# Kernel optimization log

Measured on AMD Instinct MI355X. Metric: run time of the kernel, lower is better.

The kernel has to match this reference:

```python
import jax, jax.numpy as jnp
import numpy as np

D_MODEL = 768
NUM_HEADS = 12
HEAD_DIM = D_MODEL // NUM_HEADS

def setup_inputs() -> dict:
    key = jax.random.key(0)
    ks = jax.random.split(key, 7)
    B, S = 2, 4096
    q = jax.random.normal(ks[0], (B, S, D_MODEL), dtype=jnp.float32)
    k = jax.random.normal(ks[1], (B, S, D_MODEL), dtype=jnp.float32)
    v = jax.random.normal(ks[2], (B, S, D_MODEL), dtype=jnp.float32)
    # nn.Linear(d, d, bias=False): weight [out, in], y = x @ W.T
    s = 1.0 / np.sqrt(D_MODEL)
    W_q = jax.random.uniform(ks[3], (D_MODEL, D_MODEL), jnp.float32, -s, s)
    W_k = jax.random.uniform(ks[4], (D_MODEL, D_MODEL), jnp.float32, -s, s)
    W_v = jax.random.uniform(ks[5], (D_MODEL, D_MODEL), jnp.float32, -s, s)
    W_o = jax.random.uniform(ks[6], (D_MODEL, D_MODEL), jnp.float32, -s, s)
    return {"query": q, "key": k, "value": v,
            "W_q": W_q, "W_k": W_k, "W_v": W_v, "W_o": W_o}

def reference(query, key, value, W_q, W_k, W_v, W_o):
    B, S, _ = query.shape
    H, Dh = NUM_HEADS, HEAD_DIM
    scale = np.sqrt(Dh).astype(np.float32)

    def proj(x, W):  # x [B,S,D] -> [B,H,S,Dh]
        y = jnp.einsum('bsd,ed->bse', x, W)
        return y.reshape(B, S, H, Dh).transpose(0, 2, 1, 3)

    Q = proj(query, W_q)
    K = proj(key, W_k)
    V = proj(value, W_v)
    scores = jnp.einsum('bhqd,bhkd->bhqk', Q, K) / scale
    attn = jax.nn.softmax(scores, axis=-1)  # dropout p=0 -> identity (eval)
    out = jnp.einsum('bhqk,bhkd->bhqd', attn, V)
    out = out.transpose(0, 2, 1, 3).reshape(B, S, H * Dh)
    return jnp.einsum('bsd,ed->bse', out, W_o)
```

## Files before the change

kernel.cpp:

```cpp
#include <hip/hip_runtime.h>

#define D_MODEL 768
#define S_LEN   4096
#define NHEAD   12
#define HDIM    64
#define BATCH   2
#define M_ROWS  (BATCH * S_LEN)

typedef __bf16    bf16x8 __attribute__((ext_vector_type(8)));
typedef float     f32x4  __attribute__((ext_vector_type(4)));
typedef float     f32x16 __attribute__((ext_vector_type(16)));
typedef unsigned  u32x4  __attribute__((ext_vector_type(4)));

#define QSCALE 0.18033688011f

__device__ __forceinline__ unsigned int bfb(float x) {
    return (unsigned int)__builtin_bit_cast(unsigned short, (__bf16)x);
}

__device__ __forceinline__ unsigned cvtpk(float lo, float hi) {
    unsigned r;
    asm("v_cvt_pk_bf16_f32 %0, %1, %2" : "=v"(r) : "v"(lo), "v"(hi));
    return r;
}

#if !__has_builtin(__builtin_amdgcn_exp2f)
extern "C" __device__ float __ocml_native_exp2_f32(float);
#endif
__device__ __forceinline__ float fexp2(float x) {
#if __has_builtin(__builtin_amdgcn_exp2f)
    return __builtin_amdgcn_exp2f(x);
#else
    return __ocml_native_exp2_f32(x);
#endif
}

__device__ __forceinline__ void gload16(const void* g, const void* l) {
    __builtin_amdgcn_global_load_lds(
        (const __attribute__((address_space(1))) unsigned int*)g,
        (__attribute__((address_space(3))) unsigned int*)l, 16, 0, 0);
}

#define MFMA16(a, b, c) __builtin_amdgcn_mfma_f32_16x16x32_bf16(a, b, c, 0, 0, 0)
#define MFMA32(a, b, c) __builtin_amdgcn_mfma_f32_32x32x16_bf16(a, b, c, 0, 0, 0)

__global__ __launch_bounds__(256)
void cvt_bf16(const float* __restrict__ s0, const float* __restrict__ s1,
              const float* __restrict__ s2, const float* __restrict__ s3,
              __bf16* __restrict__ d0, __bf16* __restrict__ d1,
              __bf16* __restrict__ d2, __bf16* __restrict__ d3, int n) {
    const int z = blockIdx.y;
    const float* s = z == 0 ? s0 : z == 1 ? s1 : z == 2 ? s2 : s3;
    __bf16*      d = z == 0 ? d0 : z == 1 ? d1 : z == 2 ? d2 : d3;
    const size_t i = ((size_t)blockIdx.x * 256 + threadIdx.x) * 8;
    if (i >= (size_t)n) return;
    float4 a = *(const float4*)(s + i);
    float4 b = *(const float4*)(s + i + 4);
    bf16x8 o;
    o[0] = (__bf16)a.x; o[1] = (__bf16)a.y; o[2] = (__bf16)a.z; o[3] = (__bf16)a.w;
    o[4] = (__bf16)b.x; o[5] = (__bf16)b.y; o[6] = (__bf16)b.z; o[7] = (__bf16)b.w;
    *(bf16x8*)(d + i) = o;
}

__global__ __launch_bounds__(256)
void mm_qkv(const __bf16* __restrict__ X0, const __bf16* __restrict__ X1,
            const __bf16* __restrict__ X2, const __bf16* __restrict__ W0,
            const __bf16* __restrict__ W1, const __bf16* __restrict__ W2,
            __bf16* __restrict__ C0q, __bf16* __restrict__ C1k,
            __bf16* __restrict__ C2v) {
    __shared__ __align__(16) char lds[24576];
    const int z = blockIdx.z;
    const __bf16* Xb = z == 0 ? X0 : z == 1 ? X1 : X2;
    const __bf16* Wb = z == 0 ? W0 : z == 1 ? W1 : W2;

    const int t    = threadIdx.x;
    const int w    = t >> 6;
    const int wr   = w >> 1, wc = w & 1;
    const int lane = t & 63;
    const int q15  = lane & 15;
    const int g    = lane >> 4;
    const int n0   = blockIdx.x * 64;
    const int m0   = blockIdx.y * 128;

    f32x4 acc[4][2];
#pragma unroll
    for (int i = 0; i < 4; i++)
#pragma unroll
        for (int j = 0; j < 2; j++) acc[i][j] = (f32x4){0.f, 0.f, 0.f, 0.f};

    const int srow  = lane >> 2;
    const int sslot = lane & 3;

#define MM_STAGE(B, K0)                                                        \
    {                                                                          \
        _Pragma("unroll")                                                      \
        for (int j = 0; j < 2; j++) {                                          \
            const int lrow = j * 64 + w * 16 + srow;                           \
            const int xs   = (lrow ^ (lrow >> 2)) & 3;                         \
            gload16(Xb + (size_t)(m0 + lrow) * D_MODEL + (K0) +                \
                        ((sslot ^ xs) << 3),                                   \
                    lds + (B) * 12288 + j * 4096 + w * 1024);                  \
        }                                                                      \
        {                                                                      \
            const int lrow = w * 16 + srow;                                    \
            const int xs   = (lrow ^ (lrow >> 2)) & 3;                         \
            gload16(Wb + (size_t)(n0 + lrow) * D_MODEL + (K0) +                \
                        ((sslot ^ xs) << 3),                                   \
                    lds + (B) * 12288 + 8192 + w * 1024);                      \
        }                                                                      \
    }

#define MM_COMPUTE(B)                                                          \
    {                                                                          \
        bf16x8 xa[4], wf[2];                                                   \
        _Pragma("unroll")                                                      \
        for (int mi = 0; mi < 4; mi++) {                                       \
            const int r  = wr * 64 + mi * 16 + q15;                            \
            const int sl = g ^ ((r ^ (r >> 2)) & 3);                           \
            xa[mi] = *(const bf16x8*)(lds + (B) * 12288 + r * 64 + sl * 16);   \
        }                                                                      \
        _Pragma("unroll")                                                      \
        for (int nj = 0; nj < 2; nj++) {                                       \
            const int r  = wc * 32 + nj * 16 + q15;                            \
            const int sl = g ^ ((r ^ (r >> 2)) & 3);                           \
            wf[nj] = *(const bf16x8*)(lds + (B) * 12288 + 8192 + r * 64 +      \
                                      sl * 16);                                \
        }                                                                      \
        _Pragma("unroll")                                                      \
        for (int mi = 0; mi < 4; mi++)                                         \
            _Pragma("unroll")                                                  \
            for (int nj = 0; nj < 2; nj++)                                     \
                acc[mi][nj] = MFMA16(xa[mi], wf[nj], acc[mi][nj]);             \
    }

    MM_STAGE(0, 0);
    __syncthreads();
#pragma unroll 1
    for (int ks = 0; ks < 24; ks += 2) {
        if (ks + 1 < 24) MM_STAGE(1, (ks + 1) * 32);
        MM_COMPUTE(0);
        __syncthreads();
        if (ks + 2 < 24) MM_STAGE(0, (ks + 2) * 32);
        MM_COMPUTE(1);
        __syncthreads();
    }
#undef MM_STAGE
#undef MM_COMPUTE

#pragma unroll
    for (int mi = 0; mi < 4; mi++) {
#pragma unroll
        for (int nj = 0; nj < 2; nj++) {
            const int n  = n0 + wc * 32 + nj * 16 + q15;
            const int mb = m0 + wr * 64 + mi * 16 + 4 * g;
            const int h = n >> 6, dh = n & 63;
            if (z == 0) {
#pragma unroll
                for (int r = 0; r < 4; r++) {
                    const int m = mb + r, b = m >> 12, s = m & 4095;
                    C0q[(((size_t)(b * NHEAD + h)) * S_LEN + s) * HDIM + dh] =
                        (__bf16)(acc[mi][nj][r] * QSCALE);
                }
            } else if (z == 1) {
#pragma unroll
                for (int r = 0; r < 4; r++) {
                    const int m = mb + r, b = m >> 12, s = m & 4095;
                    C1k[(((size_t)(b * NHEAD + h)) * S_LEN + s) * HDIM + dh] =
                        (__bf16)acc[mi][nj][r];
                }
            } else {
                const int b = mb >> 12, s = mb & 4095;
                uint2 pk;
                pk.x = bfb(acc[mi][nj][0]) | (bfb(acc[mi][nj][1]) << 16);
                pk.y = bfb(acc[mi][nj][2]) | (bfb(acc[mi][nj][3]) << 16);
                *(uint2*)(C2v +
                    (((size_t)(b * NHEAD + h)) * HDIM + dh) * S_LEN + s) = pk;
            }
        }
    }
}

__global__ __launch_bounds__(256)
void mm_out(const __bf16* __restrict__ Xb, const __bf16* __restrict__ Wb,
            float* __restrict__ C0) {
    __shared__ __align__(16) char lds[24576];
    const int t    = threadIdx.x;
    const int w    = t >> 6;
    const int wr   = w >> 1, wc = w & 1;
    const int lane = t & 63;
    const int q15  = lane & 15;
    const int g    = lane >> 4;
    const int n0   = blockIdx.x * 64;
    const int m0   = blockIdx.y * 128;

    f32x4 acc[4][2];
#pragma unroll
    for (int i = 0; i < 4; i++)
#pragma unroll
        for (int j = 0; j < 2; j++) acc[i][j] = (f32x4){0.f, 0.f, 0.f, 0.f};

    const int srow  = lane >> 2;
    const int sslot = lane & 3;

#define MM_STAGE(B, K0)                                                        \
    {                                                                          \
        _Pragma("unroll")                                                      \
        for (int j = 0; j < 2; j++) {                                          \
            const int lrow = j * 64 + w * 16 + srow;                           \
            const int xs   = (lrow ^ (lrow >> 2)) & 3;                         \
            gload16(Xb + (size_t)(m0 + lrow) * D_MODEL + (K0) +                \
                        ((sslot ^ xs) << 3),                                   \
                    lds + (B) * 12288 + j * 4096 + w * 1024);                  \
        }                                                                      \
        {                                                                      \
            const int lrow = w * 16 + srow;                                    \
            const int xs   = (lrow ^ (lrow >> 2)) & 3;                         \
            gload16(Wb + (size_t)(n0 + lrow) * D_MODEL + (K0) +                \
                        ((sslot ^ xs) << 3),                                   \
                    lds + (B) * 12288 + 8192 + w * 1024);                      \
        }                                                                      \
    }

#define MM_COMPUTE(B)                                                          \
    {                                                                          \
        bf16x8 xa[4], wf[2];                                                   \
        _Pragma("unroll")                                                      \
        for (int mi = 0; mi < 4; mi++) {                                       \
            const int r  = wr * 64 + mi * 16 + q15;                            \
            const int sl = g ^ ((r ^ (r >> 2)) & 3);                           \
            xa[mi] = *(const bf16x8*)(lds + (B) * 12288 + r * 64 + sl * 16);   \
        }                                                                      \
        _Pragma("unroll")                                                      \
        for (int nj = 0; nj < 2; nj++) {                                       \
            const int r  = wc * 32 + nj * 16 + q15;                            \
            const int sl = g ^ ((r ^ (r >> 2)) & 3);                           \
            wf[nj] = *(const bf16x8*)(lds + (B) * 12288 + 8192 + r * 64 +      \
                                      sl * 16);                                \
        }                                                                      \
        _Pragma("unroll")                                                      \
        for (int mi = 0; mi < 4; mi++)                                         \
            _Pragma("unroll")                                                  \
            for (int nj = 0; nj < 2; nj++)                                     \
                acc[mi][nj] = MFMA16(xa[mi], wf[nj], acc[mi][nj]);             \
    }

    MM_STAGE(0, 0);
    __syncthreads();
#pragma unroll 1
    for (int ks = 0; ks < 24; ks += 2) {
        if (ks + 1 < 24) MM_STAGE(1, (ks + 1) * 32);
        MM_COMPUTE(0);
        __syncthreads();
        if (ks + 2 < 24) MM_STAGE(0, (ks + 2) * 32);
        MM_COMPUTE(1);
        __syncthreads();
    }
#undef MM_STAGE
#undef MM_COMPUTE

#pragma unroll
    for (int mi = 0; mi < 4; mi++)
#pragma unroll
        for (int nj = 0; nj < 2; nj++) {
            const int n  = n0 + wc * 32 + nj * 16 + q15;
            const int mb = m0 + wr * 64 + mi * 16 + 4 * g;
#pragma unroll
            for (int r = 0; r < 4; r++)
                C0[(size_t)(mb + r) * D_MODEL + n] = acc[mi][nj][r];
        }
}

__global__ __launch_bounds__(256, 2)
void flash_attn(const __bf16* __restrict__ Qb, const char* __restrict__ Kb,
                const char* __restrict__ Vtb, __bf16* __restrict__ Ab) {
    __shared__ __align__(16) char lds[32768];
    const int t    = threadIdx.x;
    const int w    = t >> 6;
    const int lane = t & 63;
    const int q31  = lane & 31;
    const int hl   = lane >> 5;
    const int swz  = (q31 & 7) << 4;

    const int bid = blockIdx.x;
    const int sb  = (bid & 7) * 96 + (bid >> 3);
    const int bh  = sb >> 5;
    const int qi  = sb & 31;
    const int b   = bh / NHEAD, h = bh % NHEAD;
    const int q0  = qi * 128 + w * 32;

    const char* kbase = Kb  + (size_t)bh * (S_LEN * HDIM * 2);
    const char* vbase = Vtb + (size_t)bh * (HDIM * S_LEN * 2);

    bf16x8 qf[4];
#pragma unroll
    for (int kc = 0; kc < 4; kc++)
        qf[kc] = *(const bf16x8*)(Qb +
            ((size_t)bh * S_LEN + q0 + q31) * HDIM + kc * 16 + hl * 8);

    const bf16x8 onesv = __builtin_bit_cast(bf16x8,
        (u32x4){0x3F803F80u, 0x3F803F80u, 0x3F803F80u, 0x3F803F80u});

    f32x16 o[2], ol;
#pragma unroll
    for (int mt = 0; mt < 2; mt++)
#pragma unroll
        for (int r = 0; r < 16; r++) o[mt][r] = 0.f;
#pragma unroll
    for (int r = 0; r < 16; r++) ol[r] = 0.f;

    const int crow = lane >> 3;
    const int scb  = ((lane & 7) << 4) ^ (crow << 4);

#define STAGE(BASE, KT)                                                        \
    {                                                                          \
        _Pragma("unroll")                                                      \
        for (int j = 0; j < 2; j++) {                                          \
            const int c = 2 * w + j;                                           \
            gload16(kbase + (size_t)((KT) * 64 + c * 8 + crow) * 128 + scb,    \
                    (BASE) + c * 1024);                                        \
            gload16(vbase + (size_t)(c * 8 + crow) * (S_LEN * 2) +             \
                        (size_t)(KT) * 128 + scb,                              \
                    (BASE) + 8192 + c * 1024);                                 \
        }                                                                      \
    }

#define COMPUTE(BASE)                                                          \
    {                                                                          \
        const char* Kt = (BASE);                                               \
        const char* Vt = (BASE) + 8192;                                        \
        f32x16 sA[2];                                                          \
        _Pragma("unroll")                                                      \
        for (int mt = 0; mt < 2; mt++)                                         \
            _Pragma("unroll")                                                  \
            for (int r = 0; r < 16; r++) sA[mt][r] = 0.f;                      \
        __builtin_amdgcn_s_setprio(1);                                         \
        _Pragma("unroll")                                                      \
        for (int kc = 0; kc < 4; kc++) {                                       \
            bf16x8 kf0 = *(const bf16x8*)(Kt + q31 * 128 +                     \
                                          ((32 * kc + 16 * hl) ^ swz));        \
            bf16x8 kf1 = *(const bf16x8*)(Kt + (32 + q31) * 128 +              \
                                          ((32 * kc + 16 * hl) ^ swz));        \
            sA[0] = MFMA32(kf0, qf[kc], sA[0]);                                \
            sA[1] = MFMA32(kf1, qf[kc], sA[1]);                                \
        }                                                                      \
        __builtin_amdgcn_s_setprio(0);                                         \
        _Pragma("unroll")                                                      \
        for (int mt = 0; mt < 2; mt++)                                         \
            _Pragma("unroll")                                                  \
            for (int r = 0; r < 16; r++) sA[mt][r] = fexp2(sA[mt][r]);         \
        u32x4 pf[4];                                                           \
        _Pragma("unroll")                                                      \
        for (int mt = 0; mt < 2; mt++)                                         \
            _Pragma("unroll")                                                  \
            for (int kvc = 0; kvc < 2; kvc++) {                                \
                unsigned w0 = cvtpk(sA[mt][8*kvc+0], sA[mt][8*kvc+1]);         \
                unsigned w1 = cvtpk(sA[mt][8*kvc+2], sA[mt][8*kvc+3]);         \
                unsigned w2 = cvtpk(sA[mt][8*kvc+4], sA[mt][8*kvc+5]);         \
                unsigned w3 = cvtpk(sA[mt][8*kvc+6], sA[mt][8*kvc+7]);         \
                asm volatile("v_permlane32_swap_b32 %0, %1"                    \
                             : "+v"(w0), "+v"(w2));                            \
                asm volatile("v_permlane32_swap_b32 %0, %1"                    \
                             : "+v"(w1), "+v"(w3));                            \
                pf[mt * 2 + kvc] = (u32x4){w0, w1, w2, w3};                    \
            }                                                                  \
        __builtin_amdgcn_s_setprio(1);                                         \
        _Pragma("unroll")                                                      \
        for (int ks = 0; ks < 4; ks++)                                         \
            ol = MFMA32(onesv, __builtin_bit_cast(bf16x8, pf[ks]), ol);        \
        _Pragma("unroll")                                                      \
        for (int mtd = 0; mtd < 2; mtd++)                                      \
            _Pragma("unroll")                                                  \
            for (int ks = 0; ks < 4; ks++) {                                   \
                bf16x8 vf = *(const bf16x8*)(Vt + (32 * mtd + q31) * 128 +     \
                                             ((32 * ks + 16 * hl) ^ swz));     \
                o[mtd] = MFMA32(vf,                                            \
                    __builtin_bit_cast(bf16x8, pf[ks]), o[mtd]);               \
            }                                                                  \
        __builtin_amdgcn_s_setprio(0);                                         \
    }

    STAGE(lds, 0);
    __syncthreads();
#pragma unroll 1
    for (int kt = 0; kt < S_LEN / 64; kt += 2) {
        STAGE(lds + 16384, kt + 1);
        COMPUTE(lds);
        __syncthreads();
        if (kt + 2 < S_LEN / 64) STAGE(lds, kt + 2);
        COMPUTE(lds + 16384);
        __syncthreads();
    }
#undef STAGE
#undef COMPUTE

    const float inv  = 1.0f / ol[0];
    const int   qrow = q0 + q31;
    __bf16* orow = Ab + ((size_t)b * S_LEN + qrow) * D_MODEL + h * HDIM;
#pragma unroll
    for (int mtd = 0; mtd < 2; mtd++)
#pragma unroll
        for (int rg = 0; rg < 4; rg++) {
            const int d0 = 32 * mtd + 8 * rg + 4 * hl;
            uint2 pk;
            pk.x = cvtpk(o[mtd][rg * 4 + 0] * inv, o[mtd][rg * 4 + 1] * inv);
            pk.y = cvtpk(o[mtd][rg * 4 + 2] * inv, o[mtd][rg * 4 + 3] * inv);
            *(uint2*)(orow + d0) = pk;
        }
}

extern "C" void kernel_launch(void* const* d_in, const int* in_sizes, int n_in,
                              void* d_out, int out_size, void* d_ws, size_t ws_size,
                              hipStream_t stream) {
    const float* q  = (const float*)d_in[0];
    const float* k  = (const float*)d_in[1];
    const float* v  = (const float*)d_in[2];
    const float* Wq = (const float*)d_in[3];
    const float* Wk = (const float*)d_in[4];
    const float* Wv = (const float*)d_in[5];
    const float* Wo = (const float*)d_in[6];
    float* out = (float*)d_out;

    const size_t per = (size_t)M_ROWS * D_MODEL;
    const size_t wsz = (size_t)D_MODEL * D_MODEL;
    __bf16* ws  = (__bf16*)d_ws;
    __bf16* qb  = ws;
    __bf16* kb  = qb  + per;
    __bf16* vb  = kb  + per;
    __bf16* Wqb = vb  + per;
    __bf16* Wkb = Wqb + wsz;
    __bf16* Wvb = Wkb + wsz;
    __bf16* Wob = Wvb + wsz;
    __bf16* Qhi = Wob + wsz;
    __bf16* Kbb = Qhi + per;
    __bf16* Vtb = Kbb + per;

    cvt_bf16<<<dim3((int)(per / 2048), 3), 256, 0, stream>>>(
        q, k, v, nullptr, qb, kb, vb, nullptr, (int)per);
    cvt_bf16<<<dim3((int)(wsz / 2048), 4), 256, 0, stream>>>(
        Wq, Wk, Wv, Wo, Wqb, Wkb, Wvb, Wob, (int)wsz);

    dim3 mmg(D_MODEL / 64, M_ROWS / 128, 3);
    mm_qkv<<<mmg, 256, 0, stream>>>(qb, kb, vb, Wqb, Wkb, Wvb, Qhi, Kbb, Vtb);

    flash_attn<<<768, 256, 0, stream>>>(Qhi, (const char*)Kbb,
                                        (const char*)Vtb, qb );

    dim3 mmo(D_MODEL / 64, M_ROWS / 128);
    mm_out<<<mmo, 256, 0, stream>>>(qb, Wob, out);
}
```

Measured before the change: 225.6 us.

## Fuse fp32-to-bf16 activation conversion into QKV projection GEMM staging

```diff
diff --git a/kernel.cpp b/kernel.cpp
--- a/kernel.cpp
+++ b/kernel.cpp
@@ -63,14 +63,14 @@
 }
 
 __global__ __launch_bounds__(256)
-void mm_qkv(const __bf16* __restrict__ X0, const __bf16* __restrict__ X1,
-            const __bf16* __restrict__ X2, const __bf16* __restrict__ W0,
+void mm_qkv(const float* __restrict__ X0, const float* __restrict__ X1,
+            const float* __restrict__ X2, const __bf16* __restrict__ W0,
             const __bf16* __restrict__ W1, const __bf16* __restrict__ W2,
             __bf16* __restrict__ C0q, __bf16* __restrict__ C1k,
             __bf16* __restrict__ C2v) {
     __shared__ __align__(16) char lds[24576];
     const int z = blockIdx.z;
-    const __bf16* Xb = z == 0 ? X0 : z == 1 ? X1 : X2;
+    const float*  Xf = z == 0 ? X0 : z == 1 ? X1 : X2;
     const __bf16* Wb = z == 0 ? W0 : z == 1 ? W1 : W2;
 
     const int t    = threadIdx.x;
@@ -91,23 +91,42 @@
     const int srow  = lane >> 2;
     const int sslot = lane & 3;
 
-#define MM_STAGE(B, K0)                                                        \
-    {                                                                          \
-        _Pragma("unroll")                                                      \
-        for (int j = 0; j < 2; j++) {                                          \
-            const int lrow = j * 64 + w * 16 + srow;                           \
-            const int xs   = (lrow ^ (lrow >> 2)) & 3;                         \
-            gload16(Xb + (size_t)(m0 + lrow) * D_MODEL + (K0) +                \
-                        ((sslot ^ xs) << 3),                                   \
-                    lds + (B) * 12288 + j * 4096 + w * 1024);                  \
-        }                                                                      \
-        {                                                                      \
-            const int lrow = w * 16 + srow;                                    \
-            const int xs   = (lrow ^ (lrow >> 2)) & 3;                         \
-            gload16(Wb + (size_t)(n0 + lrow) * D_MODEL + (K0) +                \
-                        ((sslot ^ xs) << 3),                                   \
-                    lds + (B) * 12288 + 8192 + w * 1024);                      \
-        }                                                                      \
+    const int xrow0 = t >> 3;
+    const int xcol4 = t & 7;
+    const int xsub = (xcol4 & 1) * 8;
+    const int xcs  = xcol4 >> 1;
+
+    float4 xv[4];
+
+#define X_LOAD(K0)                                                             \
+    {                                                                          \
+        _Pragma("unroll")                                                      \
+        for (int j = 0; j < 4; j++)                                            \
+            xv[j] = *(const float4*)(Xf + (size_t)(m0 + xrow0 + 32 * j) *      \
+                                         D_MODEL + (K0) + 4 * xcol4);          \
+    }
+
+#define X_WRITE(B)                                                             \
+    {                                                                          \
+        _Pragma("unroll")                                                      \
+        for (int j = 0; j < 4; j++) {                                          \
+            const int r  = xrow0 + 32 * j;                                     \
+            const int xs = (r ^ (r >> 2)) & 3;                                 \
+            uint2 pw;                                                          \
+            pw.x = cvtpk(xv[j].x, xv[j].y);                                    \
+            pw.y = cvtpk(xv[j].z, xv[j].w);                                    \
+            *(uint2*)(lds + (B) * 12288 + r * 64 + ((xcs ^ xs) << 4) + xsub) = \
+                pw;                                                            \
+        }                                                                      \
+    }
+
+#define W_STAGE(B, K0)                                                         \
+    {                                                                          \
+        const int lrow = w * 16 + srow;                                        \
+        const int xs   = (lrow ^ (lrow >> 2)) & 3;                             \
+        gload16(Wb + (size_t)(n0 + lrow) * D_MODEL + (K0) +                    \
+                    ((sslot ^ xs) << 3),                                       \
+                lds + (B) * 12288 + 8192 + w * 1024);                          \
     }
 
 #define MM_COMPUTE(B)                                                          \
@@ -133,18 +152,24 @@
                 acc[mi][nj] = MFMA16(xa[mi], wf[nj], acc[mi][nj]);             \
     }
 
-    MM_STAGE(0, 0);
+    X_LOAD(0);
+    W_STAGE(0, 0);
+    X_WRITE(0);
     __syncthreads();
 #pragma unroll 1
     for (int ks = 0; ks < 24; ks += 2) {
-        if (ks + 1 < 24) MM_STAGE(1, (ks + 1) * 32);
+        if (ks + 1 < 24) { X_LOAD((ks + 1) * 32); W_STAGE(1, (ks + 1) * 32); }
         MM_COMPUTE(0);
-        __syncthreads();
-        if (ks + 2 < 24) MM_STAGE(0, (ks + 2) * 32);
+        if (ks + 1 < 24) X_WRITE(1);
+        __syncthreads();
+        if (ks + 2 < 24) { X_LOAD((ks + 2) * 32); W_STAGE(0, (ks + 2) * 32); }
         MM_COMPUTE(1);
-        __syncthreads();
-    }
-#undef MM_STAGE
+        if (ks + 2 < 24) X_WRITE(0);
+        __syncthreads();
+    }
+#undef X_LOAD
+#undef X_WRITE
+#undef W_STAGE
 #undef MM_COMPUTE
 
 #pragma unroll
@@ -423,10 +448,8 @@
     const size_t per = (size_t)M_ROWS * D_MODEL;
     const size_t wsz = (size_t)D_MODEL * D_MODEL;
     __bf16* ws  = (__bf16*)d_ws;
-    __bf16* qb  = ws;
-    __bf16* kb  = qb  + per;
-    __bf16* vb  = kb  + per;
-    __bf16* Wqb = vb  + per;
+    __bf16* Ab  = ws;
+    __bf16* Wqb = Ab  + per;
     __bf16* Wkb = Wqb + wsz;
     __bf16* Wvb = Wkb + wsz;
     __bf16* Wob = Wvb + wsz;
@@ -434,17 +457,15 @@
     __bf16* Kbb = Qhi + per;
     __bf16* Vtb = Kbb + per;
 
-    cvt_bf16<<<dim3((int)(per / 2048), 3), 256, 0, stream>>>(
-        q, k, v, nullptr, qb, kb, vb, nullptr, (int)per);
     cvt_bf16<<<dim3((int)(wsz / 2048), 4), 256, 0, stream>>>(
         Wq, Wk, Wv, Wo, Wqb, Wkb, Wvb, Wob, (int)wsz);
 
     dim3 mmg(D_MODEL / 64, M_ROWS / 128, 3);
-    mm_qkv<<<mmg, 256, 0, stream>>>(qb, kb, vb, Wqb, Wkb, Wvb, Qhi, Kbb, Vtb);
+    mm_qkv<<<mmg, 256, 0, stream>>>(q, k, v, Wqb, Wkb, Wvb, Qhi, Kbb, Vtb);
 
     flash_attn<<<768, 256, 0, stream>>>(Qhi, (const char*)Kbb,
-                                        (const char*)Vtb, qb );
+                                        (const char*)Vtb, Ab);
 
     dim3 mmo(D_MODEL / 64, M_ROWS / 128);
-    mm_out<<<mmo, 256, 0, stream>>>(qb, Wob, out);
-}
+    mm_out<<<mmo, 256, 0, stream>>>(Ab, Wob, out);
+}
```

After: 245.5 us. 1.09x slower.
